# Optimization experiments

Measured on AMD Instinct MI355X. Metric: run time of the kernel, lower is better.

Reference implementation:

```python
import jax, jax.numpy as jnp
import numpy as np

B, T, N, F_, KH, D, KD = 16, 12, 325, 64, 4, 16, 3  # batch, time, nodes, feat, heads, head_dim, diffusion steps
H = KH // 2
EPS = 1e-5


def setup_inputs() -> dict:
    key = jax.random.key(0)
    ks = jax.random.split(key, 16)
    lin = lambda k: (jax.random.normal(k, (F_, F_), jnp.float32) * 0.02)
    return {
        "x": jax.random.normal(ks[0], (B, T, N, F_), jnp.float32),
        "A": jax.random.uniform(ks[1], (KD, N, N), jnp.float32),
        "AT": jax.random.uniform(ks[2], (KD, N, N), jnp.float32),
        "Wq": lin(ks[3]), "bq": jnp.zeros((F_,), jnp.float32),
        "Wk": lin(ks[4]), "bk": jnp.zeros((F_,), jnp.float32),
        "Wks": lin(ks[5]), "bks": jnp.zeros((F_,), jnp.float32),
        "Wv": lin(ks[6]), "bv": jnp.zeros((F_,), jnp.float32),
        "Wvs": lin(ks[7]), "bvs": jnp.zeros((F_,), jnp.float32),
        "Wdi": jax.random.normal(ks[8], (H, KD, N, N), jnp.float32) * 0.05,
        "Wdo": jax.random.normal(ks[9], (H, KD, N, N), jnp.float32) * 0.05,
        "Wf1": lin(ks[10]), "bf1": jnp.zeros((F_,), jnp.float32),
        "Wf2": lin(ks[11]), "bf2": jnp.zeros((F_,), jnp.float32),
        "g_ln": jnp.ones((F_,), jnp.float32), "b_ln": jnp.zeros((F_,), jnp.float32),
    }


def _heads(y):
    # [B,T,N,F] -> [KH,B,T,N,D]  (torch.split along -1 then stack on dim 0)
    return y.reshape(B, T, N, KH, D).transpose(3, 0, 1, 2, 4)


def _attn_half(q, k, ks_, v, vs, bias):
    # q,k,ks_,v,vs: [H,B,T,N,D]; bias: [H,1,1,N,N]
    scale = 1.0 / jnp.sqrt(jnp.float32(D))
    e = jnp.einsum('hbtnd,hbtmd->hbtnm', q, k) * scale + bias
    es = jax.nn.sigmoid((q * ks_).sum(-1, keepdims=True) * scale)  # [H,B,T,N,1]
    e = e - e.max(-1, keepdims=True)
    ex = jnp.exp(e)
    a = ex / (es + ex.sum(-1, keepdims=True))  # sigmoid-augmented softmax
    out = jnp.einsum('hbtnm,hbtmd->hbtnd', a, v)
    return out + vs - a.sum(-1, keepdims=True) * vs


def reference(x, A, AT, Wq, bq, Wk, bk, Wks, bks, Wv, bv, Wvs, bvs,
              Wdi, Wdo, Wf1, bf1, Wf2, bf2, g_ln, b_ln):
    q = _heads(x @ Wq.T + bq)
    k = _heads(x @ Wk.T + bk)
    ks_ = _heads(x @ Wks.T + bks)
    v = _heads(x @ Wv.T + bv)
    vs = _heads(x @ Wvs.T + bvs)

    # DCN graph-diffusion bias: sum_j W[h,j] * A[j] -> [H,1,1,N,N]
    bias_i = jnp.einsum('hknm,knm->hnm', Wdi, A)[:, None, None]
    bias_o = jnp.einsum('hknm,knm->hnm', Wdo, AT)[:, None, None]

    vi = _attn_half(q[:H], k[:H], ks_[:H], v[:H], vs[:H], bias_i)
    vo = _attn_half(q[H:], k[H:], ks_[H:], v[H:], vs[H:], bias_o)

    val = jnp.concatenate([vi, vo], 0)  # [KH,B,T,N,D]
    val = val.transpose(1, 2, 3, 0, 4).reshape(B, T, N, F_)

    h = jax.nn.gelu(val @ Wf1.T + bf1, approximate=False) @ Wf2.T + bf2
    h = h + x

    mu = h.mean(-1, keepdims=True)
    var = ((h - mu) ** 2).mean(-1, keepdims=True)
    return g_ln * (h - mu) / jnp.sqrt(var + EPS) + b_ln
```

## Files before the change

kernel.cpp:

```cpp
#include <hip/hip_runtime.h>
#include <hip/hip_bf16.h>
#include <math.h>

#define NN 325
#define FD 64
#define KH 4
#define DH 16
#define BT 192
#define NN2 (NN*NN)
#define PST (NN*DH)
#define WSL 5632
#define HSTR 72
#define NPROJ 975
#define NBIAS 1848
#define NPAD  (KH*BT)
#define ANB   4032
#define LOG2E 1.44269504088896f

typedef __attribute__((ext_vector_type(8))) short short8;
typedef __attribute__((ext_vector_type(4))) float f32x4;

union U8 { uint4 u; short8 s; ushort us[8]; };
__device__ inline short8 lds8(const ushort* p){ U8 t; t.u = *(const uint4*)p; return t.s; }
__device__ inline float b2f(ushort v){ return __uint_as_float(((unsigned)v) << 16); }
__device__ inline ushort f2b(float f){
  unsigned u = __float_as_uint(f);
  u += 0x7fff + ((u >> 16) & 1);
  return (ushort)(u >> 16);
}
__device__ inline unsigned pk2(float a, float b){
  union { __hip_bfloat162 h; unsigned u; } t;
  t.h = __float22bfloat162_rn(float2{a, b});
  return t.u;
}
__device__ inline short8 cvt8(const float* p){
  float4 u = ((const float4*)p)[0], v = ((const float4*)p)[1];
  U8 t;
  t.us[0]=f2b(u.x); t.us[1]=f2b(u.y); t.us[2]=f2b(u.z); t.us[3]=f2b(u.w);
  t.us[4]=f2b(v.x); t.us[5]=f2b(v.y); t.us[6]=f2b(v.z); t.us[7]=f2b(v.w);
  return t.s;
}

__global__ __launch_bounds__(256) void wpack_kernel(
    const float* __restrict__ Wq,  const float* __restrict__ bq,
    const float* __restrict__ Wk,  const float* __restrict__ bk,
    const float* __restrict__ Wks, const float* __restrict__ bks,
    const float* __restrict__ Wv,  const float* __restrict__ bv,
    const float* __restrict__ Wvs, const float* __restrict__ bvs,
    const float* __restrict__ Wf1, const float* __restrict__ Wf2,
    ushort* __restrict__ Wcat, float* __restrict__ bcat){
  int blk = blockIdx.x;
  const float* Ws[7] = {Wq, Wk, Wks, Wv, Wvs, Wf1, Wf2};
  const float* bs[5] = {bq, bk, bks, bv, bvs};
  int f = blk * 64 + (threadIdx.x >> 2);
  int c0 = (threadIdx.x & 3) * 8;
  const float* wr = Ws[blk] + (f & 63) * 64;
  unsigned* dst = (unsigned*)Wcat + f * 32 + c0;
  #pragma unroll
  for (int c = 0; c < 8; ++c)
    dst[c] = f2b(wr[2*(c0+c)]) | ((unsigned)f2b(wr[2*(c0+c)+1]) << 16);
  if (blk < 5 && (threadIdx.x & 3) == 0) bcat[f] = bs[blk][f & 63];
}

__global__ __launch_bounds__(256) void prep_kernel(
    const float* __restrict__ x, const ushort* __restrict__ Wcat,
    const float* __restrict__ bcat, ushort* __restrict__ proj,
    ushort* __restrict__ vt, ushort* __restrict__ kperm,
    const float* __restrict__ Wdi, const float* __restrict__ Wdo,
    const float* __restrict__ A,   const float* __restrict__ AT,
    ushort* __restrict__ biasB){
  int bid = blockIdx.x, tid = threadIdx.x;
  if (bid < NPROJ){
    int lane = tid & 63, wid = tid >> 6;
    int r0 = bid * 64 + wid * 16;
    int m = lane & 15, g = lane >> 4;
    int gr = r0 + m;
    int bt = gr / NN, n = gr - bt * NN;
    const float* xr = x + (size_t)gr * 64 + g * 8;
    short8 xb0 = cvt8(xr);
    short8 xb1 = cvt8(xr + 32);
    for (int ct = 0; ct < 20; ++ct){
      short8 w0 = lds8(Wcat + ((size_t)(ct*16 + m) * 64 + g * 8));
      short8 w1 = lds8(Wcat + ((size_t)(ct*16 + m) * 64 + g * 8 + 32));
      float4 b4 = *(const float4*)(bcat + ct*16 + 4*g);
      f32x4 acc = {b4.x, b4.y, b4.z, b4.w};
      acc = __builtin_amdgcn_mfma_f32_16x16x32_bf16(w0, xb0, acc, 0, 0, 0);
      acc = __builtin_amdgcn_mfma_f32_16x16x32_bf16(w1, xb1, acc, 0, 0, 0);
      if (ct >= 4 && ct < 8){
        int w = n & 31;
        ushort* kd = kperm + (size_t)((ct-4)*BT + bt) * WSL
                   + (n >> 5)*512 + ((w >> 2) & 1)*256
                   + (4*(w >> 3) + (w & 3))*16 + 4*g;
        uint2 wv; wv.x = pk2(acc[0], acc[1]); wv.y = pk2(acc[2], acc[3]);
        *(uint2*)kd = wv;
      } else if (ct >= 12 && ct < 16){
        ushort* vs = vt + (size_t)((ct-12)*BT + bt) * WSL + (n >> 5)*512 + (n & 31);
        #pragma unroll
        for (int rg = 0; rg < 4; ++rg)
          vs[(4*g + rg) * 32] = f2b(acc[rg]);
      } else {
        int slot = (ct < 4) ? ct : (ct < 12 ? ct - 4 : ct - 8);
        float sc = (ct < 4) ? 0.25f * LOG2E : 1.0f;
        uint2 w2;
        w2.x = pk2(acc[0]*sc, acc[1]*sc);
        w2.y = pk2(acc[2]*sc, acc[3]*sc);
        *(uint2*)(proj + ((size_t)slot * BT + bt) * PST + n*16 + 4*g) = w2;
      }
    }
  } else if (bid < NPROJ + NBIAS){
    int idx = (bid - NPROJ) * 256 + tid;
    int h = idx / 118272;
    int rem = idx - h * 118272;
    int qt = rem / 5632;
    int r2 = rem - qt * 5632;
    int tt = r2 >> 9, r3 = r2 & 511;
    int mq = r3 >> 5, w = r3 & 31;
    int n = qt*16 + mq;
    int tok = tt*32 + w;
    float s = -1e30f;
    if (n < NN && tok < NN){
      int ridx = n * NN + tok;
      s = 0.f;
      if (h < 2){
        #pragma unroll
        for (int k = 0; k < 3; ++k) s += Wdi[(h*3 + k)*NN2 + ridx] * A[k*NN2 + ridx];
      } else {
        int h2 = h - 2;
        #pragma unroll
        for (int k = 0; k < 3; ++k) s += Wdo[(h2*3 + k)*NN2 + ridx] * AT[k*NN2 + ridx];
      }
      s *= LOG2E;
    }
    biasB[idx] = f2b(s);
  } else {
    int slice = bid - NPROJ - NBIAS;
    if (tid < 432){
      int d = tid / 27, wz = 5 + tid % 27;
      vt[(size_t)slice * WSL + 5120 + d*32 + wz] = 0;
      int half = (wz >> 2) & 1, rr = 4*(wz >> 3) + (wz & 3);
      kperm[(size_t)slice * WSL + 5120 + half*256 + rr*16 + d] = 0;
    }
  }
}

__global__ __launch_bounds__(256, 4) void attn_kernel(
    const ushort* __restrict__ proj, const ushort* __restrict__ biasB,
    const ushort* __restrict__ vt, const ushort* __restrict__ kperm,
    ushort* __restrict__ val){
  int tid = threadIdx.x, lane = tid & 63, wid = tid >> 6;
  int bid = (int)blockIdx.x;
  int swz = (bid & 7) * (ANB/8) + (bid >> 3);
  int tile = swz * 4 + wid;
  int qt = tile % 21, bh = tile / 21;
  int h = bh / BT, bt = bh - h * BT;
  int m = lane & 15, g = lane >> 4;

  const ushort* qb  = proj + (size_t)((0*KH + h)*BT + bt) * PST;
  const ushort* ksb = proj + (size_t)((1*KH + h)*BT + bt) * PST;
  const ushort* vsb = proj + (size_t)((2*KH + h)*BT + bt) * PST;
  const ushort* kpb = kperm + (size_t)(h*BT + bt) * WSL;
  const ushort* vtb = vt    + (size_t)(h*BT + bt) * WSL;
  const ushort* bbb = biasB + (size_t)(h*21 + qt) * WSL;

  short8 zero = {0,0,0,0,0,0,0,0};
  short8 qf = (g < 2) ? lds8(qb + (size_t)(qt*16 + m)*16 + (g&1)*8) : zero;

  const ushort* ka = kpb + m*16 + (g&1)*8;
  const ushort* ba = bbb + m*32 + g*8;
  const ushort* va = vtb + m*32 + g*8;

  int nq = qt*16 + m, nb = min(nq, NN-1);
  uint2 qw = *(const uint2*)(qb + (size_t)nb*16 + g*4);
  uint2 kw = *(const uint2*)(ksb + (size_t)nb*16 + g*4);

  short8 aE[2], aO[2], bf[2], vf[2];
  aE[0] = lds8(ka);       aO[0] = lds8(ka + 256);
  bf[0] = lds8(ba);       vf[0] = lds8(va);
  aE[1] = lds8(ka + 512); aO[1] = lds8(ka + 768);
  bf[1] = lds8(ba + 512); vf[1] = lds8(va + 512);

  f32x4 o = {0.f, 0.f, 0.f, 0.f};
  float rowsum = 0.f;
  #pragma unroll
  for (int tt = 0; tt < 11; ++tt){
    const int cur = tt & 1;
    short8 aEc = aE[cur], aOc = aO[cur], bfc = bf[cur], vfc = vf[cur];
    if (tt + 2 < 11){
      aE[cur] = lds8(ka + (tt+2)*512);
      aO[cur] = lds8(ka + (tt+2)*512 + 256);
      bf[cur] = lds8(ba + (tt+2)*512);
      vf[cur] = lds8(va + (tt+2)*512);
    }
    f32x4 accE = {0.f,0.f,0.f,0.f}, accO = {0.f,0.f,0.f,0.f};
    accE = __builtin_amdgcn_mfma_f32_16x16x32_bf16(aEc, qf, accE, 0, 0, 0);
    accO = __builtin_amdgcn_mfma_f32_16x16x32_bf16(aOc, qf, accO, 0, 0, 0);
    U8 bu; bu.s = bfc;
    float e0 = __builtin_amdgcn_exp2f(accE[0] + b2f(bu.us[0]));
    float e1 = __builtin_amdgcn_exp2f(accE[1] + b2f(bu.us[1]));
    float e2 = __builtin_amdgcn_exp2f(accE[2] + b2f(bu.us[2]));
    float e3 = __builtin_amdgcn_exp2f(accE[3] + b2f(bu.us[3]));
    float e4 = __builtin_amdgcn_exp2f(accO[0] + b2f(bu.us[4]));
    float e5 = __builtin_amdgcn_exp2f(accO[1] + b2f(bu.us[5]));
    float e6 = __builtin_amdgcn_exp2f(accO[2] + b2f(bu.us[6]));
    float e7 = __builtin_amdgcn_exp2f(accO[3] + b2f(bu.us[7]));
    rowsum += ((e0 + e1) + (e2 + e3)) + ((e4 + e5) + (e6 + e7));
    U8 pf;
    pf.u.x = pk2(e0, e1);
    pf.u.y = pk2(e2, e3);
    pf.u.z = pk2(e4, e5);
    pf.u.w = pk2(e6, e7);
    o = __builtin_amdgcn_mfma_f32_16x16x32_bf16(pf.s, vfc, o, 0, 0, 0);
  }

  rowsum += __shfl_xor(rowsum, 16, 64);
  rowsum += __shfl_xor(rowsum, 32, 64);

  float dp = b2f((ushort)(qw.x & 0xffff)) * b2f((ushort)(kw.x & 0xffff))
           + b2f((ushort)(qw.x >> 16))    * b2f((ushort)(kw.x >> 16))
           + b2f((ushort)(qw.y & 0xffff)) * b2f((ushort)(kw.y & 0xffff))
           + b2f((ushort)(qw.y >> 16))    * b2f((ushort)(kw.y >> 16));
  dp += __shfl_xor(dp, 16, 64);
  dp += __shfl_xor(dp, 32, 64);
  float esv  = __builtin_amdgcn_rcpf(1.f + __builtin_amdgcn_exp2f(-dp));
  float inv  = __builtin_amdgcn_rcpf(esv + rowsum);
  float beta = 1.f - rowsum * inv;

  int sb = g << 4;
  float invr[4], betr[4];
  #pragma unroll
  for (int rg = 0; rg < 4; ++rg){
    invr[rg] = __uint_as_float(__builtin_amdgcn_ds_bpermute(sb + rg*4, __float_as_uint(inv)));
    betr[rg] = __uint_as_float(__builtin_amdgcn_ds_bpermute(sb + rg*4, __float_as_uint(beta)));
  }
  #pragma unroll
  for (int rg = 0; rg < 4; ++rg){
    int n = qt*16 + 4*g + rg;
    int nc = min(n, NN-1);
    float vsx = b2f(vsb[(size_t)nc*16 + m]);
    float res = o[rg]*invr[rg] + betr[rg]*vsx;
    if (n < NN) val[((size_t)bt*NN + n)*FD + h*16 + m] = f2b(res);
  }
}

__global__ __launch_bounds__(256) void ffn_kernel(
    const ushort* __restrict__ val, const float* __restrict__ x,
    const ushort* __restrict__ Wf1b, const float* __restrict__ bf1,
    const ushort* __restrict__ Wf2b, const float* __restrict__ bf2,
    const float* __restrict__ g_ln, const float* __restrict__ b_ln,
    float* __restrict__ out){
  __shared__ ushort hs[4][16 * HSTR];
  int tid = threadIdx.x, lane = tid & 63, wid = tid >> 6;
  int m = lane & 15, g = lane >> 4;
  int r0 = blockIdx.x * 64 + wid * 16;
  int row = r0 + m;

  short8 vb0 = lds8(val + ((size_t)row * 64 + g * 8));
  short8 vb1 = lds8(val + ((size_t)row * 64 + g * 8 + 32));

  #pragma unroll
  for (int ct = 0; ct < 4; ++ct){
    short8 w0 = lds8(Wf1b + ((size_t)(ct*16 + m) * 64 + g * 8));
    short8 w1 = lds8(Wf1b + ((size_t)(ct*16 + m) * 64 + g * 8 + 32));
    float4 b4 = *(const float4*)(bf1 + ct*16 + 4*g);
    f32x4 acc = {b4.x, b4.y, b4.z, b4.w};
    acc = __builtin_amdgcn_mfma_f32_16x16x32_bf16(w0, vb0, acc, 0, 0, 0);
    acc = __builtin_amdgcn_mfma_f32_16x16x32_bf16(w1, vb1, acc, 0, 0, 0);
    uint2 w;
    float g0 = 0.5f*acc[0]*(1.f + erff(acc[0]*0.70710678118654752f));
    float g1 = 0.5f*acc[1]*(1.f + erff(acc[1]*0.70710678118654752f));
    float g2 = 0.5f*acc[2]*(1.f + erff(acc[2]*0.70710678118654752f));
    float g3 = 0.5f*acc[3]*(1.f + erff(acc[3]*0.70710678118654752f));
    w.x = pk2(g0, g1); w.y = pk2(g2, g3);
    *(uint2*)&hs[wid][m * HSTR + ct*16 + 4*g] = w;
  }
  asm volatile("s_waitcnt lgkmcnt(0)" ::: "memory");
  short8 h0 = lds8(&hs[wid][m * HSTR + g * 8]);
  short8 h1 = lds8(&hs[wid][m * HSTR + g * 8 + 32]);

  float t[4][4];
  #pragma unroll
  for (int ct = 0; ct < 4; ++ct){
    short8 w0 = lds8(Wf2b + ((size_t)(ct*16 + m) * 64 + g * 8));
    short8 w1 = lds8(Wf2b + ((size_t)(ct*16 + m) * 64 + g * 8 + 32));
    float4 b4 = *(const float4*)(bf2 + ct*16 + 4*g);
    f32x4 acc = {b4.x, b4.y, b4.z, b4.w};
    acc = __builtin_amdgcn_mfma_f32_16x16x32_bf16(w0, h0, acc, 0, 0, 0);
    acc = __builtin_amdgcn_mfma_f32_16x16x32_bf16(w1, h1, acc, 0, 0, 0);
    float4 xr = *(const float4*)(x + (size_t)row * 64 + ct*16 + 4*g);
    t[ct][0] = acc[0] + xr.x; t[ct][1] = acc[1] + xr.y;
    t[ct][2] = acc[2] + xr.z; t[ct][3] = acc[3] + xr.w;
  }
  float s = 0.f;
  #pragma unroll
  for (int ct = 0; ct < 4; ++ct) s += (t[ct][0]+t[ct][1]) + (t[ct][2]+t[ct][3]);
  s += __shfl_xor(s, 16, 64); s += __shfl_xor(s, 32, 64);
  float mu = s * (1.f/64.f);
  float v = 0.f;
  #pragma unroll
  for (int ct = 0; ct < 4; ++ct){
    #pragma unroll
    for (int rg = 0; rg < 4; ++rg){ float d = t[ct][rg] - mu; v += d*d; }
  }
  v += __shfl_xor(v, 16, 64); v += __shfl_xor(v, 32, 64);
  float rs = rsqrtf(v * (1.f/64.f) + 1e-5f);
  #pragma unroll
  for (int ct = 0; ct < 4; ++ct){
    float4 g4 = *(const float4*)(g_ln + ct*16 + 4*g);
    float4 bb = *(const float4*)(b_ln + ct*16 + 4*g);
    float4 o;
    o.x = g4.x*(t[ct][0]-mu)*rs + bb.x;
    o.y = g4.y*(t[ct][1]-mu)*rs + bb.y;
    o.z = g4.z*(t[ct][2]-mu)*rs + bb.z;
    o.w = g4.w*(t[ct][3]-mu)*rs + bb.w;
    *(float4*)(out + (size_t)row * 64 + ct*16 + 4*g) = o;
  }
}

extern "C" void kernel_launch(void* const* d_in, const int* in_sizes, int n_in,
                              void* d_out, int out_size, void* d_ws, size_t ws_size,
                              hipStream_t stream) {
  const float* x    = (const float*)d_in[0];
  const float* A    = (const float*)d_in[1];
  const float* AT   = (const float*)d_in[2];
  const float* Wq   = (const float*)d_in[3];
  const float* bq   = (const float*)d_in[4];
  const float* Wk   = (const float*)d_in[5];
  const float* bk   = (const float*)d_in[6];
  const float* Wks  = (const float*)d_in[7];
  const float* bks  = (const float*)d_in[8];
  const float* Wv   = (const float*)d_in[9];
  const float* bv   = (const float*)d_in[10];
  const float* Wvs  = (const float*)d_in[11];
  const float* bvs  = (const float*)d_in[12];
  const float* Wdi  = (const float*)d_in[13];
  const float* Wdo  = (const float*)d_in[14];
  const float* Wf1  = (const float*)d_in[15];
  const float* bf1  = (const float*)d_in[16];
  const float* Wf2  = (const float*)d_in[17];
  const float* bf2  = (const float*)d_in[18];
  const float* g_ln = (const float*)d_in[19];
  const float* b_ln = (const float*)d_in[20];
  float* out = (float*)d_out;

  float* ws = (float*)d_ws;
  ushort* proj  = (ushort*)ws;
  ushort* biasB = (ushort*)(ws + 5990400);
  ushort* val   = (ushort*)(ws + 6226944);
  ushort* vt    = (ushort*)(ws + 8223744);
  ushort* kperm = (ushort*)(ws + 10386432);
  ushort* Wcat  = (ushort*)(ws + 12549120);
  float*  bcat  = ws + 12563456;
  ushort* Wf1b  = Wcat + 320*64;
  ushort* Wf2b  = Wcat + 384*64;

  wpack_kernel<<<7, 256, 0, stream>>>(Wq, bq, Wk, bk, Wks, bks,
                                      Wv, bv, Wvs, bvs, Wf1, Wf2, Wcat, bcat);
  prep_kernel<<<NPROJ + NBIAS + NPAD, 256, 0, stream>>>(
      x, Wcat, bcat, proj, vt, kperm, Wdi, Wdo, A, AT, biasB);
  attn_kernel<<<ANB, 256, 0, stream>>>(proj, biasB, vt, kperm, val);
  ffn_kernel<<<975, 256, 0, stream>>>(val, x, Wf1b, bf1, Wf2b, bf2,
                                      g_ln, b_ln, out);
}
```

Before: 190.0 us.

## Process two query tiles per wave, fold fp32 bias into MFMA accumulator

Each wave now handles two 16-row query tiles and reuses the same K and V fragments for both, which halves the K/V loads per query and the number of blocks. The diffusion bias is stored as fp32 in MFMA accumulator layout and passed in as the initial accumulator, so the per-element bf16 unpack and add go away. Row sums come from an extra MFMA against a vector of ones, and the final normalization is reformulated. In exchange the bias buffer doubles in size, register pressure rises (occupancy lowered to 3), and prefetching is reduced from two stages to one.

Result: no change. 188.6 us (-0.7%).

```diff
diff --git a/kernel.cpp b/kernel.cpp
--- a/kernel.cpp
+++ b/kernel.cpp
@@ -14,7 +14,7 @@
 #define NPROJ 975
 #define NBIAS 1848
 #define NPAD  (KH*BT)
-#define ANB   4032
+#define ANB   2112
 #define LOG2E 1.44269504088896f
 
 typedef __attribute__((ext_vector_type(8))) short short8;
@@ -68,7 +68,7 @@
     ushort* __restrict__ vt, ushort* __restrict__ kperm,
     const float* __restrict__ Wdi, const float* __restrict__ Wdo,
     const float* __restrict__ A,   const float* __restrict__ AT,
-    ushort* __restrict__ biasB){
+    float* __restrict__ biasF){
   int bid = blockIdx.x, tid = threadIdx.x;
   if (bid < NPROJ){
     int lane = tid & 63, wid = tid >> 6;
@@ -114,9 +114,9 @@
     int qt = rem / 5632;
     int r2 = rem - qt * 5632;
     int tt = r2 >> 9, r3 = r2 & 511;
-    int mq = r3 >> 5, w = r3 & 31;
-    int n = qt*16 + mq;
-    int tok = tt*32 + w;
+    int gg = r3 >> 7, mm = (r3 >> 3) & 15, e8 = r3 & 7;
+    int n = qt*16 + mm;
+    int tok = tt*32 + gg*8 + e8;
     float s = -1e30f;
     if (n < NN && tok < NN){
       int ridx = n * NN + tok;
@@ -131,7 +131,7 @@
       }
       s *= LOG2E;
     }
-    biasB[idx] = f2b(s);
+    biasF[idx] = s;
   } else {
     int slice = bid - NPROJ - NBIAS;
     if (tid < 432){
@@ -143,102 +143,123 @@
   }
 }
 
-__global__ __launch_bounds__(256, 4) void attn_kernel(
-    const ushort* __restrict__ proj, const ushort* __restrict__ biasB,
+__global__ __launch_bounds__(256, 3) void attn_kernel(
+    const ushort* __restrict__ proj, const float* __restrict__ biasF,
     const ushort* __restrict__ vt, const ushort* __restrict__ kperm,
     ushort* __restrict__ val){
   int tid = threadIdx.x, lane = tid & 63, wid = tid >> 6;
   int bid = (int)blockIdx.x;
   int swz = (bid & 7) * (ANB/8) + (bid >> 3);
-  int tile = swz * 4 + wid;
-  int qt = tile % 21, bh = tile / 21;
+  int p = swz * 4 + wid;
+  int j = p % 11, bh = p / 11;
   int h = bh / BT, bt = bh - h * BT;
+  int qt1 = 2*j;
+  int two = (j < 10);
+  int qt2 = two ? qt1 + 1 : qt1;
   int m = lane & 15, g = lane >> 4;
 
   const ushort* qb  = proj + (size_t)((0*KH + h)*BT + bt) * PST;
   const ushort* ksb = proj + (size_t)((1*KH + h)*BT + bt) * PST;
   const ushort* vsb = proj + (size_t)((2*KH + h)*BT + bt) * PST;
-  const ushort* kpb = kperm + (size_t)(h*BT + bt) * WSL;
-  const ushort* vtb = vt    + (size_t)(h*BT + bt) * WSL;
-  const ushort* bbb = biasB + (size_t)(h*21 + qt) * WSL;
+  const ushort* ka  = kperm + (size_t)(h*BT + bt) * WSL + m*16 + (g&1)*8;
+  const ushort* va  = vt    + (size_t)(h*BT + bt) * WSL + m*32 + g*8;
+  const float*  b1a = biasF + (size_t)(h*21 + qt1) * WSL + g*128 + m*8;
+  const float*  b2a = biasF + (size_t)(h*21 + qt2) * WSL + g*128 + m*8;
 
   short8 zero = {0,0,0,0,0,0,0,0};
-  short8 qf = (g < 2) ? lds8(qb + (size_t)(qt*16 + m)*16 + (g&1)*8) : zero;
-
-  const ushort* ka = kpb + m*16 + (g&1)*8;
-  const ushort* ba = bbb + m*32 + g*8;
-  const ushort* va = vtb + m*32 + g*8;
-
-  int nq = qt*16 + m, nb = min(nq, NN-1);
-  uint2 qw = *(const uint2*)(qb + (size_t)nb*16 + g*4);
-  uint2 kw = *(const uint2*)(ksb + (size_t)nb*16 + g*4);
-
-  short8 aE[2], aO[2], bf[2], vf[2];
-  aE[0] = lds8(ka);       aO[0] = lds8(ka + 256);
-  bf[0] = lds8(ba);       vf[0] = lds8(va);
-  aE[1] = lds8(ka + 512); aO[1] = lds8(ka + 768);
-  bf[1] = lds8(ba + 512); vf[1] = lds8(va + 512);
-
-  f32x4 o = {0.f, 0.f, 0.f, 0.f};
-  float rowsum = 0.f;
+  short8 qf1 = (g < 2) ? lds8(qb + (size_t)(qt1*16 + m)*16 + (g&1)*8) : zero;
+  short8 qf2 = (g < 2) ? lds8(qb + (size_t)(qt2*16 + m)*16 + (g&1)*8) : zero;
+
+  int nb1 = min(qt1*16 + m, NN-1), nb2 = min(qt2*16 + m, NN-1);
+  uint2 qw1 = *(const uint2*)(qb  + (size_t)nb1*16 + g*4);
+  uint2 kw1 = *(const uint2*)(ksb + (size_t)nb1*16 + g*4);
+  uint2 qw2 = *(const uint2*)(qb  + (size_t)nb2*16 + g*4);
+  uint2 kw2 = *(const uint2*)(ksb + (size_t)nb2*16 + g*4);
+
+  short8 kE = lds8(ka), kO = lds8(ka + 256), vv = lds8(va);
+  f32x4 bE1 = *(const f32x4*)(b1a), bO1 = *(const f32x4*)(b1a + 4);
+  f32x4 bE2 = *(const f32x4*)(b2a), bO2 = *(const f32x4*)(b2a + 4);
+
+  short8 ones = {16256,16256,16256,16256,16256,16256,16256,16256};
+  f32x4 o1 = {0.f,0.f,0.f,0.f}, o2 = {0.f,0.f,0.f,0.f};
+  f32x4 r1 = {0.f,0.f,0.f,0.f}, r2 = {0.f,0.f,0.f,0.f};
+
   #pragma unroll
   for (int tt = 0; tt < 11; ++tt){
-    const int cur = tt & 1;
-    short8 aEc = aE[cur], aOc = aO[cur], bfc = bf[cur], vfc = vf[cur];
-    if (tt + 2 < 11){
-      aE[cur] = lds8(ka + (tt+2)*512);
-      aO[cur] = lds8(ka + (tt+2)*512 + 256);
-      bf[cur] = lds8(ba + (tt+2)*512);
-      vf[cur] = lds8(va + (tt+2)*512);
-    }
-    f32x4 accE = {0.f,0.f,0.f,0.f}, accO = {0.f,0.f,0.f,0.f};
-    accE = __builtin_amdgcn_mfma_f32_16x16x32_bf16(aEc, qf, accE, 0, 0, 0);
-    accO = __builtin_amdgcn_mfma_f32_16x16x32_bf16(aOc, qf, accO, 0, 0, 0);
-    U8 bu; bu.s = bfc;
-    float e0 = __builtin_amdgcn_exp2f(accE[0] + b2f(bu.us[0]));
-    float e1 = __builtin_amdgcn_exp2f(accE[1] + b2f(bu.us[1]));
-    float e2 = __builtin_amdgcn_exp2f(accE[2] + b2f(bu.us[2]));
-    float e3 = __builtin_amdgcn_exp2f(accE[3] + b2f(bu.us[3]));
-    float e4 = __builtin_amdgcn_exp2f(accO[0] + b2f(bu.us[4]));
-    float e5 = __builtin_amdgcn_exp2f(accO[1] + b2f(bu.us[5]));
-    float e6 = __builtin_amdgcn_exp2f(accO[2] + b2f(bu.us[6]));
-    float e7 = __builtin_amdgcn_exp2f(accO[3] + b2f(bu.us[7]));
-    rowsum += ((e0 + e1) + (e2 + e3)) + ((e4 + e5) + (e6 + e7));
-    U8 pf;
-    pf.u.x = pk2(e0, e1);
-    pf.u.y = pk2(e2, e3);
-    pf.u.z = pk2(e4, e5);
-    pf.u.w = pk2(e6, e7);
-    o = __builtin_amdgcn_mfma_f32_16x16x32_bf16(pf.s, vfc, o, 0, 0, 0);
-  }
-
-  rowsum += __shfl_xor(rowsum, 16, 64);
-  rowsum += __shfl_xor(rowsum, 32, 64);
-
-  float dp = b2f((ushort)(qw.x & 0xffff)) * b2f((ushort)(kw.x & 0xffff))
-           + b2f((ushort)(qw.x >> 16))    * b2f((ushort)(kw.x >> 16))
-           + b2f((ushort)(qw.y & 0xffff)) * b2f((ushort)(kw.y & 0xffff))
-           + b2f((ushort)(qw.y >> 16))    * b2f((ushort)(kw.y >> 16));
-  dp += __shfl_xor(dp, 16, 64);
-  dp += __shfl_xor(dp, 32, 64);
-  float esv  = __builtin_amdgcn_rcpf(1.f + __builtin_amdgcn_exp2f(-dp));
-  float inv  = __builtin_amdgcn_rcpf(esv + rowsum);
-  float beta = 1.f - rowsum * inv;
-
+    short8 kEn = zero, kOn = zero, vvn = zero;
+    f32x4 bE1n = bE1, bO1n = bO1, bE2n = bE2, bO2n = bO2;
+    if (tt < 10){
+      const ushort* kan = ka + (tt+1)*512;
+      kEn  = lds8(kan); kOn = lds8(kan + 256);
+      vvn  = lds8(va + (tt+1)*512);
+      bE1n = *(const f32x4*)(b1a + (tt+1)*512);
+      bO1n = *(const f32x4*)(b1a + (tt+1)*512 + 4);
+      bE2n = *(const f32x4*)(b2a + (tt+1)*512);
+      bO2n = *(const f32x4*)(b2a + (tt+1)*512 + 4);
+    }
+    f32x4 aE1 = __builtin_amdgcn_mfma_f32_16x16x32_bf16(kE, qf1, bE1, 0, 0, 0);
+    f32x4 aO1 = __builtin_amdgcn_mfma_f32_16x16x32_bf16(kO, qf1, bO1, 0, 0, 0);
+    float e0 = __builtin_amdgcn_exp2f(aE1[0]);
+    float e1 = __builtin_amdgcn_exp2f(aE1[1]);
+    float e2 = __builtin_amdgcn_exp2f(aE1[2]);
+    float e3 = __builtin_amdgcn_exp2f(aE1[3]);
+    float e4 = __builtin_amdgcn_exp2f(aO1[0]);
+    float e5 = __builtin_amdgcn_exp2f(aO1[1]);
+    float e6 = __builtin_amdgcn_exp2f(aO1[2]);
+    float e7 = __builtin_amdgcn_exp2f(aO1[3]);
+    U8 p1;
+    p1.u.x = pk2(e0, e1); p1.u.y = pk2(e2, e3);
+    p1.u.z = pk2(e4, e5); p1.u.w = pk2(e6, e7);
+    o1 = __builtin_amdgcn_mfma_f32_16x16x32_bf16(p1.s, vv,   o1, 0, 0, 0);
+    r1 = __builtin_amdgcn_mfma_f32_16x16x32_bf16(p1.s, ones, r1, 0, 0, 0);
+    f32x4 aE2 = __builtin_amdgcn_mfma_f32_16x16x32_bf16(kE, qf2, bE2, 0, 0, 0);
+    f32x4 aO2 = __builtin_amdgcn_mfma_f32_16x16x32_bf16(kO, qf2, bO2, 0, 0, 0);
+    float f0 = __builtin_amdgcn_exp2f(aE2[0]);
+    float f1 = __builtin_amdgcn_exp2f(aE2[1]);
+    float f2 = __builtin_amdgcn_exp2f(aE2[2]);
+    float f3 = __builtin_amdgcn_exp2f(aE2[3]);
+    float f4 = __builtin_amdgcn_exp2f(aO2[0]);
+    float f5 = __builtin_amdgcn_exp2f(aO2[1]);
+    float f6 = __builtin_amdgcn_exp2f(aO2[2]);
+    float f7 = __builtin_amdgcn_exp2f(aO2[3]);
+    U8 p2;
+    p2.u.x = pk2(f0, f1); p2.u.y = pk2(f2, f3);
+    p2.u.z = pk2(f4, f5); p2.u.w = pk2(f6, f7);
+    o2 = __builtin_amdgcn_mfma_f32_16x16x32_bf16(p2.s, vv,   o2, 0, 0, 0);
+    r2 = __builtin_amdgcn_mfma_f32_16x16x32_bf16(p2.s, ones, r2, 0, 0, 0);
+    kE = kEn; kO = kOn; vv = vvn;
+    bE1 = bE1n; bO1 = bO1n; bE2 = bE2n; bO2 = bO2n;
+  }
+
+  float dp1 = b2f((ushort)(qw1.x & 0xffff)) * b2f((ushort)(kw1.x & 0xffff))
+            + b2f((ushort)(qw1.x >> 16))    * b2f((ushort)(kw1.x >> 16))
+            + b2f((ushort)(qw1.y & 0xffff)) * b2f((ushort)(kw1.y & 0xffff))
+            + b2f((ushort)(qw1.y >> 16))    * b2f((ushort)(kw1.y >> 16));
+  float dp2 = b2f((ushort)(qw2.x & 0xffff)) * b2f((ushort)(kw2.x & 0xffff))
+            + b2f((ushort)(qw2.x >> 16))    * b2f((ushort)(kw2.x >> 16))
+            + b2f((ushort)(qw2.y & 0xffff)) * b2f((ushort)(kw2.y & 0xffff))
+            + b2f((ushort)(qw2.y >> 16))    * b2f((ushort)(kw2.y >> 16));
+  dp1 += __shfl_xor(dp1, 16, 64); dp1 += __shfl_xor(dp1, 32, 64);
+  dp2 += __shfl_xor(dp2, 16, 64); dp2 += __shfl_xor(dp2, 32, 64);
   int sb = g << 4;
-  float invr[4], betr[4];
   #pragma unroll
   for (int rg = 0; rg < 4; ++rg){
-    invr[rg] = __uint_as_float(__builtin_amdgcn_ds_bpermute(sb + rg*4, __float_as_uint(inv)));
-    betr[rg] = __uint_as_float(__builtin_amdgcn_ds_bpermute(sb + rg*4, __float_as_uint(beta)));
-  }
-  #pragma unroll
-  for (int rg = 0; rg < 4; ++rg){
-    int n = qt*16 + 4*g + rg;
-    int nc = min(n, NN-1);
-    float vsx = b2f(vsb[(size_t)nc*16 + m]);
-    float res = o[rg]*invr[rg] + betr[rg]*vsx;
-    if (n < NN) val[((size_t)bt*NN + n)*FD + h*16 + m] = f2b(res);
+    float d1 = __uint_as_float(__builtin_amdgcn_ds_bpermute(sb + rg*4, __float_as_uint(dp1)));
+    float d2 = __uint_as_float(__builtin_amdgcn_ds_bpermute(sb + rg*4, __float_as_uint(dp2)));
+    float es1 = __builtin_amdgcn_rcpf(1.f + __builtin_amdgcn_exp2f(-d1));
+    float es2 = __builtin_amdgcn_rcpf(1.f + __builtin_amdgcn_exp2f(-d2));
+    int n1 = qt1*16 + 4*g + rg;
+    int n2 = qt2*16 + 4*g + rg;
+    float vsx1 = b2f(vsb[(size_t)min(n1, NN-1)*16 + m]);
+    float vsx2 = b2f(vsb[(size_t)min(n2, NN-1)*16 + m]);
+    float iv1 = __builtin_amdgcn_rcpf(es1 + r1[rg]);
+    float res1 = (o1[rg] + es1 * vsx1) * iv1;
+    if (n1 < NN) val[((size_t)bt*NN + n1)*FD + h*16 + m] = f2b(res1);
+    if (two){
+      float iv2 = __builtin_amdgcn_rcpf(es2 + r2[rg]);
+      float res2 = (o2[rg] + es2 * vsx2) * iv2;
+      if (n2 < NN) val[((size_t)bt*NN + n2)*FD + h*16 + m] = f2b(res2);
+    }
   }
 }
 
@@ -344,20 +365,20 @@
 
   float* ws = (float*)d_ws;
   ushort* proj  = (ushort*)ws;
-  ushort* biasB = (ushort*)(ws + 5990400);
-  ushort* val   = (ushort*)(ws + 6226944);
-  ushort* vt    = (ushort*)(ws + 8223744);
-  ushort* kperm = (ushort*)(ws + 10386432);
-  ushort* Wcat  = (ushort*)(ws + 12549120);
-  float*  bcat  = ws + 12563456;
+  float*  biasF = ws + 5990400;
+  ushort* val   = (ushort*)(ws + 6463488);
+  ushort* vt    = (ushort*)(ws + 8460288);
+  ushort* kperm = (ushort*)(ws + 10622976);
+  ushort* Wcat  = (ushort*)(ws + 12785664);
+  float*  bcat  = ws + 12800000;
   ushort* Wf1b  = Wcat + 320*64;
   ushort* Wf2b  = Wcat + 384*64;
 
   wpack_kernel<<<7, 256, 0, stream>>>(Wq, bq, Wk, bk, Wks, bks,
                                       Wv, bv, Wvs, bvs, Wf1, Wf2, Wcat, bcat);
   prep_kernel<<<NPROJ + NBIAS + NPAD, 256, 0, stream>>>(
-      x, Wcat, bcat, proj, vt, kperm, Wdi, Wdo, A, AT, biasB);
-  attn_kernel<<<ANB, 256, 0, stream>>>(proj, biasB, vt, kperm, val);
+      x, Wcat, bcat, proj, vt, kperm, Wdi, Wdo, A, AT, biasF);
+  attn_kernel<<<ANB, 256, 0, stream>>>(proj, biasF, vt, kperm, val);
   ffn_kernel<<<975, 256, 0, stream>>>(val, x, Wf1b, bf1, Wf2b, bf2,
                                       g_ln, b_ln, out);
 }
```
